# Performance work log

Measured on AMD Instinct MI355X. Metric: run time of the kernel, lower is better.

## Reference

```python
import jax, jax.numpy as jnp
import numpy as np
from jax.scipy.special import logsumexp

EPSILON = 0.01        # temperature
DIST_THRESH = 0.2
NUM_ITERS = 3
NEG_INF = -1.0e9

B, N, M, C = 4, 4096, 4096, 256


def setup_inputs() -> dict:
    key = jax.random.key(0)
    k1, k2, k3, k4, k5 = jax.random.split(key, 5)
    source_feats = jax.random.normal(k1, (B, N, C), dtype=jnp.float32)
    source_locs = jax.random.uniform(k2, (B, N, 2), dtype=jnp.float32)
    target_locs = jax.random.uniform(k3, (B, M, 2), dtype=jnp.float32)
    source_valid_mask = jax.random.bernoulli(k4, 0.9, (B, N))
    target_valid_mask = jax.random.bernoulli(k5, 0.9, (B, M))
    return {
        "source_feats": source_feats,
        "source_locs": source_locs,
        "target_locs": target_locs,
        "source_valid_mask": source_valid_mask,
        "target_valid_mask": target_valid_mask,
    }


def reference(source_feats, source_locs, target_locs, source_valid_mask, target_valid_mask):
    # pairwise squared distances: [B, M, N]
    diff = target_locs[:, :, None, :] - source_locs[:, None, :, :]  # [B, M, N, 2]
    dist_sq = jnp.sum(diff * diff, axis=-1)                          # [B, M, N]
    log_K = -dist_sq / (EPSILON + 1e-8)

    valid_connection = dist_sq < (DIST_THRESH ** 2)
    valid_connection = valid_connection & source_valid_mask[:, None, :]
    valid_connection = valid_connection & target_valid_mask[:, :, None]
    log_K = jnp.where(valid_connection, log_K, NEG_INF)

    # Sinkhorn iterations in log space
    v = jnp.zeros((log_K.shape[0], 1, log_K.shape[2]), dtype=log_K.dtype)  # [B,1,N]
    u = jnp.zeros((log_K.shape[0], log_K.shape[1], 1), dtype=log_K.dtype)  # [B,M,1]
    for _ in range(NUM_ITERS):
        u = -logsumexp(log_K + v, axis=2, keepdims=True)
        v = -logsumexp(log_K + u, axis=1, keepdims=True)
        v = jnp.where(source_valid_mask[:, None, :], v, 0.0)

    attn = jnp.exp(log_K + u + v)  # [B, M, N]
    attn = jax.lax.stop_gradient(attn)  # original computes it under torch.no_grad

    target_feats = jnp.einsum('bmn,bnc->bmc', attn, source_feats)
    target_feats = target_feats * target_valid_mask[:, :, None].astype(target_feats.dtype)
    has_source = jnp.any(valid_connection, axis=-1, keepdims=True)
    target_feats = target_feats * has_source.astype(target_feats.dtype)
    return target_feats
```

## Files before the change

kernel.cpp:

```cpp
#include <hip/hip_runtime.h>
#include <math.h>

#define BB 4
#define BN 4096
#define CC 256
constexpr float T2      = 0.04f;
constexpr float NEGINF  = -1.0e9f;
constexpr float INV_EPS = (float)(1.0 / 0.01000001);

__device__ __forceinline__ int cell_of(float x, float y) {
  int cx = (int)(x * 5.0f); cx = cx < 0 ? 0 : (cx > 4 ? 4 : cx);
  int cy = (int)(y * 5.0f); cy = cy < 0 ? 0 : (cy > 4 ? 4 : cy);
  return cy * 5 + cx;
}

__global__ void k_count(const float* __restrict__ tlocs, const float* __restrict__ slocs,
                        int* __restrict__ counts_t, int* __restrict__ counts_s) {
  int gid = blockIdx.x * 256 + threadIdx.x;
  if (gid < BB * BN) {
    int b = gid >> 12;
    atomicAdd(&counts_t[b * 32 + cell_of(tlocs[gid * 2], tlocs[gid * 2 + 1])], 1);
  } else {
    int g = gid - BB * BN;
    int b = g >> 12;
    atomicAdd(&counts_s[b * 32 + cell_of(slocs[g * 2], slocs[g * 2 + 1])], 1);
  }
}

__global__ void k_scan_scatter(const float* __restrict__ tlocs, const float* __restrict__ slocs,
                               const int* __restrict__ tmask, const int* __restrict__ smask,
                               const int* __restrict__ counts_t, const int* __restrict__ counts_s,
                               int* __restrict__ starts_t, int* __restrict__ starts_s,
                               int* __restrict__ perm_t, int* __restrict__ perm_s,
                               float4* __restrict__ t_sorted, float4* __restrict__ s_sorted) {
  const int which = blockIdx.x & 1, b = blockIdx.x >> 1;
  const float* locs = which ? slocs : tlocs;
  const int*   mask = which ? smask : tmask;
  const int* counts = which ? counts_s : counts_t;
  int* starts       = which ? starts_s : starts_t;
  int* perm         = which ? perm_s : perm_t;
  float4* pack      = which ? s_sorted : t_sorted;
  __shared__ int st[26];
  __shared__ int cur[25];
  if (threadIdx.x == 0) {
    int acc = 0;
    for (int c = 0; c < 25; c++) { st[c] = acc; acc += counts[b * 32 + c]; }
    st[25] = acc;
  }
  __syncthreads();
  if (threadIdx.x < 25) cur[threadIdx.x] = st[threadIdx.x];
  if (threadIdx.x < 26) starts[b * 32 + threadIdx.x] = st[threadIdx.x];
  __syncthreads();
  for (int i = threadIdx.x; i < BN; i += 256) {
    float x = locs[(b * BN + i) * 2], y = locs[(b * BN + i) * 2 + 1];
    int pos = atomicAdd(&cur[cell_of(x, y)], 1);
    perm[b * BN + pos] = i;
    pack[b * BN + pos] = make_float4(x, y, 0.f, mask[b * BN + i] ? 1.f : 0.f);
  }
}

__global__ __launch_bounds__(256) void k_sink(const float4* __restrict__ opp,
                                              float4* __restrict__ own,
                                              const int* __restrict__ opp_starts,
                                              const int* __restrict__ Zin,
                                              int* __restrict__ Zout,
                                              int zero_invalid) {
  const int wv   = threadIdx.x >> 6;
  const int lane = threadIdx.x & 63;
  const int rowb = blockIdx.x * 16 + wv * 4;
  const int b    = rowb >> 12;
  float4 me[4];
  float  s[4] = {0.f, 0.f, 0.f, 0.f};
  int ryLo = 5, ryHi = -1, rxLo = 5, rxHi = -1;
  #pragma unroll
  for (int i = 0; i < 4; i++) {
    me[i] = own[rowb + i];
    if (me[i].w != 0.f) {
      int cell = cell_of(me[i].x, me[i].y);
      int cy = cell / 5, cx = cell % 5;
      ryLo = min(ryLo, max(cy - 1, 0)); ryHi = max(ryHi, min(cy + 1, 4));
      rxLo = min(rxLo, max(cx - 1, 0)); rxHi = max(rxHi, min(cx + 1, 4));
    }
  }
  for (int ry = ryLo; ry <= ryHi; ry++) {
    const int r0 = opp_starts[b * 32 + ry * 5 + rxLo];
    const int r1 = opp_starts[b * 32 + ry * 5 + rxHi + 1];
    for (int j = r0 + lane; j < r1; j += 64) {
      float4 o = opp[b * BN + j];
      #pragma unroll
      for (int i = 0; i < 4; i++) {
        float dx = me[i].x - o.x, dy = me[i].y - o.y;
        float d2 = fmaf(dx, dx, dy * dy);
        bool  c  = (d2 < T2) && (o.w != 0.f) && (me[i].w != 0.f);
        float t  = c ? fmaf(d2, -INV_EPS, o.z) : -3e30f;
        s[i] += __expf(t);
      }
    }
  }
  #pragma unroll
  for (int i = 0; i < 4; i++)
    for (int off = 32; off > 0; off >>= 1) s[i] += __shfl_xor(s[i], off);
  if (lane == 0) {
    const float Zf = (float)Zin[b];
    #pragma unroll
    for (int i = 0; i < 4; i++) {
      float ss  = s[i] + Zf;
      float val = (ss > 0.f) ? -logf(ss) : 1.0e9f;
      if (zero_invalid && me[i].w == 0.f) val = 0.f;
      own[rowb + i] = make_float4(me[i].x, me[i].y, val, me[i].w);
      if (val == 1.0e9f) atomicAdd(&Zout[b], 1);
    }
  }
}

#define MAXCH 12

__global__ __launch_bounds__(256) void k_out(
    const float* __restrict__ feats, const float4* __restrict__ t_sorted,
    const float4* __restrict__ s_sorted, const int* __restrict__ perm_t,
    const int* __restrict__ perm_s, const int* __restrict__ starts_t,
    const int* __restrict__ starts_s, float* __restrict__ out) {
  const int b = blockIdx.z;
  const int cell = blockIdx.y / 3, rsel = blockIdx.y % 3;
  const int cy = cell / 5, cx = cell % 5;
  const int ry = cy + rsel - 1;
  if (ry < 0 || ry > 4) return;
  const int t0 = starts_t[b * 32 + cell], t1 = starts_t[b * 32 + cell + 1];
  const int base = t0 + blockIdx.x * 32;
  if (base >= t1) return;
  const int rx0 = max(cx - 1, 0), rx1 = min(cx + 1, 4);
  const int s0 = starts_s[b * 32 + ry * 5 + rx0];
  const int s1 = starts_s[b * 32 + ry * 5 + rx1 + 1];
  if (s0 >= s1) return;
  const int nt = min(32, t1 - base);

  __shared__ float4 tL[32];
  __shared__ int    morg[32];
  __shared__ float4 sL[16];
  __shared__ int    sorg[16];
  __shared__ __align__(16) float attnL[16][32];
  __shared__ __align__(16) float fL[16 * 256];

  const int tid = threadIdx.x;
  if (tid < 32) {
    if (tid < nt) {
      tL[tid]   = t_sorted[b * BN + base + tid];
      morg[tid] = perm_t[b * BN + base + tid];
    } else {
      tL[tid]   = make_float4(0.f, 0.f, 0.f, 0.f);
      morg[tid] = 0;
    }
  }
  const int tmg = tid >> 5;
  const int chg = tid & 31;
  float acc[4][8];
  #pragma unroll
  for (int i = 0; i < 4; i++)
    #pragma unroll
    for (int j = 0; j < 8; j++) acc[i][j] = 0.f;
  __syncthreads();

  for (int n0 = s0; n0 < s1; n0 += 16) {
    const int kk = min(16, s1 - n0);
    __syncthreads();
    if (tid < 16) {
      if (tid < kk) {
        sL[tid]   = s_sorted[b * BN + n0 + tid];
        sorg[tid] = perm_s[b * BN + n0 + tid];
      } else {
        sL[tid]   = make_float4(1e9f, 1e9f, 0.f, 0.f);
        sorg[tid] = 0;
      }
    }
    __syncthreads();
    {
      int e = tid * 2;
      #pragma unroll
      for (int q = 0; q < 2; q++, e++) {
        int nn = e >> 5, tm = e & 31;
        float4 t4 = tL[tm];
        float4 s4 = sL[nn];
        float dx = t4.x - s4.x, dy = t4.y - s4.y;
        float d2 = fmaf(dx, dx, dy * dy);
        bool  c  = (d2 < T2) && (s4.w != 0.f) && (t4.w != 0.f);
        attnL[nn][tm] = c ? __expf(fmaf(d2, -INV_EPS, t4.z + s4.z)) : 0.f;
      }
    }
    #pragma unroll
    for (int q = 0; q < 4; q++) {
      int idx = q * 256 + tid;
      ((float4*)fL)[idx] =
          ((const float4*)feats)[(((b << 12) + sorg[idx >> 6]) << 6) + (idx & 63)];
    }
    __syncthreads();
    #pragma unroll 4
    for (int nn = 0; nn < 16; nn++) {
      const float4 av = *(const float4*)&attnL[nn][tmg * 4];
      const float4 f0 = *(const float4*)&fL[nn * 256 + chg * 4];
      const float4 f1 = *(const float4*)&fL[nn * 256 + 128 + chg * 4];
      float avv[4] = {av.x, av.y, av.z, av.w};
      float ff[8]  = {f0.x, f0.y, f0.z, f0.w, f1.x, f1.y, f1.z, f1.w};
      #pragma unroll
      for (int i = 0; i < 4; i++)
        #pragma unroll
        for (int j = 0; j < 8; j++)
          acc[i][j] = fmaf(avv[i], ff[j], acc[i][j]);
    }
  }
  __syncthreads();
  #pragma unroll
  for (int i = 0; i < 4; i++) {
    int tm = tmg * 4 + i;
    if (tm < nt) {
      float* op = out + (((b << 12) + morg[tm]) << 8) + chg * 4;
      #pragma unroll
      for (int j = 0; j < 4; j++) atomicAdd(op + j,       acc[i][j]);
      #pragma unroll
      for (int j = 0; j < 4; j++) atomicAdd(op + 128 + j, acc[i][j + 4]);
    }
  }
}

extern "C" void kernel_launch(void* const* d_in, const int* in_sizes, int n_in,
                              void* d_out, int out_size, void* d_ws, size_t ws_size,
                              hipStream_t stream) {
  const float* feats = (const float*)d_in[0];
  const float* slocs = (const float*)d_in[1];
  const float* tlocs = (const float*)d_in[2];
  const int*   smask = (const int*)d_in[3];
  const int*   tmask = (const int*)d_in[4];
  float* out = (float*)d_out;

  char* ws = (char*)d_ws;
  int*    counts_t = (int*)(ws);
  int*    counts_s = (int*)(ws + 512);
  int*    Zc       = (int*)(ws + 1024);
  int*    starts_t = (int*)(ws + 2048);
  int*    starts_s = (int*)(ws + 2560);
  int*    perm_t   = (int*)(ws + 4096);
  int*    perm_s   = (int*)(ws + 69632);
  float4* s_sorted = (float4*)(ws + 135168);
  float4* t_sorted = (float4*)(ws + 397312);

  hipMemsetAsync(ws, 0, 2048, stream);
  hipMemsetAsync(out, 0, (size_t)out_size * sizeof(float), stream);
  k_count<<<128, 256, 0, stream>>>(tlocs, slocs, counts_t, counts_s);
  k_scan_scatter<<<8, 256, 0, stream>>>(tlocs, slocs, tmask, smask,
                                        counts_t, counts_s, starts_t, starts_s,
                                        perm_t, perm_s, t_sorted, s_sorted);
  for (int it = 0; it < 3; it++) {
    k_sink<<<1024, 256, 0, stream>>>(s_sorted, t_sorted, starts_s,
                                     Zc + (it == 0 ? 0 : (2 * it) * 4),
                                     Zc + (2 * it + 1) * 4, 0);
    k_sink<<<1024, 256, 0, stream>>>(t_sorted, s_sorted, starts_t,
                                     Zc + (2 * it + 1) * 4,
                                     Zc + (2 * it + 2) * 4, 1);
  }
  k_out<<<dim3(MAXCH, 75, BB), 256, 0, stream>>>(feats, t_sorted, s_sorted,
                                                 perm_t, perm_s, starts_t,
                                                 starts_s, out);
}
```

Baseline: 598.8 us.

## Fuse counting, scatter and Sinkhorn passes into one cooperative kernel

Replaces the count, scan/scatter and six Sinkhorn launches (plus a workspace memset) with a single cooperative kernel that uses grid-wide syncs between phases. This removes per-launch overhead and inter-kernel gaps. In exchange it needs all 1024 blocks co-resident for the cooperative launch, and the grid syncs add their own barrier cost. The scatter phase now runs on only 8 of the 1024 blocks while the rest wait.

```diff
diff --git a/kernel.cpp b/kernel.cpp
--- a/kernel.cpp
+++ b/kernel.cpp
@@ -1,5 +1,8 @@
 #include <hip/hip_runtime.h>
+#include <hip/hip_cooperative_groups.h>
 #include <math.h>
+
+namespace cg = cooperative_groups;
 
 #define BB 4
 #define BN 4096
@@ -14,57 +17,12 @@
   return cy * 5 + cx;
 }
 
-__global__ void k_count(const float* __restrict__ tlocs, const float* __restrict__ slocs,
-                        int* __restrict__ counts_t, int* __restrict__ counts_s) {
-  int gid = blockIdx.x * 256 + threadIdx.x;
-  if (gid < BB * BN) {
-    int b = gid >> 12;
-    atomicAdd(&counts_t[b * 32 + cell_of(tlocs[gid * 2], tlocs[gid * 2 + 1])], 1);
-  } else {
-    int g = gid - BB * BN;
-    int b = g >> 12;
-    atomicAdd(&counts_s[b * 32 + cell_of(slocs[g * 2], slocs[g * 2 + 1])], 1);
-  }
-}
-
-__global__ void k_scan_scatter(const float* __restrict__ tlocs, const float* __restrict__ slocs,
-                               const int* __restrict__ tmask, const int* __restrict__ smask,
-                               const int* __restrict__ counts_t, const int* __restrict__ counts_s,
-                               int* __restrict__ starts_t, int* __restrict__ starts_s,
-                               int* __restrict__ perm_t, int* __restrict__ perm_s,
-                               float4* __restrict__ t_sorted, float4* __restrict__ s_sorted) {
-  const int which = blockIdx.x & 1, b = blockIdx.x >> 1;
-  const float* locs = which ? slocs : tlocs;
-  const int*   mask = which ? smask : tmask;
-  const int* counts = which ? counts_s : counts_t;
-  int* starts       = which ? starts_s : starts_t;
-  int* perm         = which ? perm_s : perm_t;
-  float4* pack      = which ? s_sorted : t_sorted;
-  __shared__ int st[26];
-  __shared__ int cur[25];
-  if (threadIdx.x == 0) {
-    int acc = 0;
-    for (int c = 0; c < 25; c++) { st[c] = acc; acc += counts[b * 32 + c]; }
-    st[25] = acc;
-  }
-  __syncthreads();
-  if (threadIdx.x < 25) cur[threadIdx.x] = st[threadIdx.x];
-  if (threadIdx.x < 26) starts[b * 32 + threadIdx.x] = st[threadIdx.x];
-  __syncthreads();
-  for (int i = threadIdx.x; i < BN; i += 256) {
-    float x = locs[(b * BN + i) * 2], y = locs[(b * BN + i) * 2 + 1];
-    int pos = atomicAdd(&cur[cell_of(x, y)], 1);
-    perm[b * BN + pos] = i;
-    pack[b * BN + pos] = make_float4(x, y, 0.f, mask[b * BN + i] ? 1.f : 0.f);
-  }
-}
-
-__global__ __launch_bounds__(256) void k_sink(const float4* __restrict__ opp,
-                                              float4* __restrict__ own,
-                                              const int* __restrict__ opp_starts,
-                                              const int* __restrict__ Zin,
-                                              int* __restrict__ Zout,
-                                              int zero_invalid) {
+__device__ static void sink_pass(const float4* __restrict__ opp,
+                                 float4* __restrict__ own,
+                                 const int* __restrict__ opp_starts,
+                                 const int* __restrict__ Zin,
+                                 int* __restrict__ Zout,
+                                 int zero_invalid) {
   const int wv   = threadIdx.x >> 6;
   const int lane = threadIdx.x & 63;
   const int rowb = blockIdx.x * 16 + wv * 4;
@@ -110,6 +68,78 @@
       own[rowb + i] = make_float4(me[i].x, me[i].y, val, me[i].w);
       if (val == 1.0e9f) atomicAdd(&Zout[b], 1);
     }
+  }
+}
+
+__global__ __launch_bounds__(256) void k_fused(
+    const float* __restrict__ tlocs, const float* __restrict__ slocs,
+    const int* __restrict__ tmask, const int* __restrict__ smask,
+    int* __restrict__ wsi,
+    int* __restrict__ starts_t, int* __restrict__ starts_s,
+    int* __restrict__ perm_t, int* __restrict__ perm_s,
+    float4* __restrict__ t_sorted, float4* __restrict__ s_sorted) {
+  cg::grid_group grid = cg::this_grid();
+  int* counts_t = wsi;
+  int* counts_s = wsi + 128;
+  int* Zc       = wsi + 256;
+  const int tid  = threadIdx.x;
+  const int gtid = blockIdx.x * 256 + tid;
+
+  if (gtid < 512) wsi[gtid] = 0;
+  __threadfence();
+  grid.sync();
+
+  if (gtid < 2 * BB * BN) {
+    if (gtid < BB * BN) {
+      int b = gtid >> 12;
+      atomicAdd(&counts_t[b * 32 + cell_of(tlocs[gtid * 2], tlocs[gtid * 2 + 1])], 1);
+    } else {
+      int g = gtid - BB * BN;
+      int b = g >> 12;
+      atomicAdd(&counts_s[b * 32 + cell_of(slocs[g * 2], slocs[g * 2 + 1])], 1);
+    }
+  }
+  __threadfence();
+  grid.sync();
+
+  __shared__ int st[26];
+  __shared__ int cur[25];
+  if (blockIdx.x < 8) {
+    const int which = blockIdx.x & 1, b = blockIdx.x >> 1;
+    const float* locs = which ? slocs : tlocs;
+    const int*   mask = which ? smask : tmask;
+    const int* counts = which ? counts_s : counts_t;
+    int* starts       = which ? starts_s : starts_t;
+    int* perm         = which ? perm_s : perm_t;
+    float4* pack      = which ? s_sorted : t_sorted;
+    if (tid == 0) {
+      int acc = 0;
+      for (int c = 0; c < 25; c++) { st[c] = acc; acc += counts[b * 32 + c]; }
+      st[25] = acc;
+    }
+    __syncthreads();
+    if (tid < 25) cur[tid] = st[tid];
+    if (tid < 26) starts[b * 32 + tid] = st[tid];
+    __syncthreads();
+    for (int i = tid; i < BN; i += 256) {
+      float x = locs[(b * BN + i) * 2], y = locs[(b * BN + i) * 2 + 1];
+      int pos = atomicAdd(&cur[cell_of(x, y)], 1);
+      perm[b * BN + pos] = i;
+      pack[b * BN + pos] = make_float4(x, y, 0.f, mask[b * BN + i] ? 1.f : 0.f);
+    }
+  }
+  __threadfence();
+  grid.sync();
+
+  for (int it = 0; it < 3; it++) {
+    sink_pass(s_sorted, t_sorted, starts_s,
+              Zc + (it == 0 ? 0 : (2 * it) * 4), Zc + (2 * it + 1) * 4, 0);
+    __threadfence();
+    grid.sync();
+    sink_pass(t_sorted, s_sorted, starts_t,
+              Zc + (2 * it + 1) * 4, Zc + (2 * it + 2) * 4, 1);
+    __threadfence();
+    grid.sync();
   }
 }
 
@@ -232,9 +262,7 @@
   float* out = (float*)d_out;
 
   char* ws = (char*)d_ws;
-  int*    counts_t = (int*)(ws);
-  int*    counts_s = (int*)(ws + 512);
-  int*    Zc       = (int*)(ws + 1024);
+  int*    wsi      = (int*)(ws);
   int*    starts_t = (int*)(ws + 2048);
   int*    starts_s = (int*)(ws + 2560);
   int*    perm_t   = (int*)(ws + 4096);
@@ -242,20 +270,14 @@
   float4* s_sorted = (float4*)(ws + 135168);
   float4* t_sorted = (float4*)(ws + 397312);
 
-  hipMemsetAsync(ws, 0, 2048, stream);
   hipMemsetAsync(out, 0, (size_t)out_size * sizeof(float), stream);
-  k_count<<<128, 256, 0, stream>>>(tlocs, slocs, counts_t, counts_s);
-  k_scan_scatter<<<8, 256, 0, stream>>>(tlocs, slocs, tmask, smask,
-                                        counts_t, counts_s, starts_t, starts_s,
-                                        perm_t, perm_s, t_sorted, s_sorted);
-  for (int it = 0; it < 3; it++) {
-    k_sink<<<1024, 256, 0, stream>>>(s_sorted, t_sorted, starts_s,
-                                     Zc + (it == 0 ? 0 : (2 * it) * 4),
-                                     Zc + (2 * it + 1) * 4, 0);
-    k_sink<<<1024, 256, 0, stream>>>(t_sorted, s_sorted, starts_t,
-                                     Zc + (2 * it + 1) * 4,
-                                     Zc + (2 * it + 2) * 4, 1);
-  }
+
+  void* kargs[] = {(void*)&tlocs, (void*)&slocs, (void*)&tmask, (void*)&smask,
+                   (void*)&wsi, (void*)&starts_t, (void*)&starts_s,
+                   (void*)&perm_t, (void*)&perm_s,
+                   (void*)&t_sorted, (void*)&s_sorted};
+  hipLaunchCooperativeKernel(k_fused, dim3(1024), dim3(256), kargs, 0, stream);
+
   k_out<<<dim3(MAXCH, 75, BB), 256, 0, stream>>>(feats, t_sorted, s_sorted,
                                                  perm_t, perm_s, starts_t,
                                                  starts_s, out);
```

Result: slower. 2.073 ms (+246.2%).

## Double-buffer feature tiles with async global-to-LDS loads and fuse binning kernels

Applied to the files above, without the earlier changes.

The output kernel now double-buffers source feature rows in LDS, using global_load_lds DMA and register prefetch of the next tile's locations and permutation indices, so loads overlap the FMA accumulation. The attention tile is padded and computed directly from registers. The count and scan/scatter kernels merge into one kernel that does per-batch shared-memory counting and also zeroes Zc, which removes one launch and a memset. The cost is extra LDS (two feature buffers), which may lower occupancy, and added complexity in waitcnt and barrier handling.

```diff
diff --git a/kernel.cpp b/kernel.cpp
--- a/kernel.cpp
+++ b/kernel.cpp
@@ -5,7 +5,6 @@
 #define BN 4096
 #define CC 256
 constexpr float T2      = 0.04f;
-constexpr float NEGINF  = -1.0e9f;
 constexpr float INV_EPS = (float)(1.0 / 0.01000001);
 
 __device__ __forceinline__ int cell_of(float x, float y) {
@@ -14,44 +13,45 @@
   return cy * 5 + cx;
 }
 
-__global__ void k_count(const float* __restrict__ tlocs, const float* __restrict__ slocs,
-                        int* __restrict__ counts_t, int* __restrict__ counts_s) {
-  int gid = blockIdx.x * 256 + threadIdx.x;
-  if (gid < BB * BN) {
-    int b = gid >> 12;
-    atomicAdd(&counts_t[b * 32 + cell_of(tlocs[gid * 2], tlocs[gid * 2 + 1])], 1);
-  } else {
-    int g = gid - BB * BN;
-    int b = g >> 12;
-    atomicAdd(&counts_s[b * 32 + cell_of(slocs[g * 2], slocs[g * 2 + 1])], 1);
-  }
-}
-
-__global__ void k_scan_scatter(const float* __restrict__ tlocs, const float* __restrict__ slocs,
-                               const int* __restrict__ tmask, const int* __restrict__ smask,
-                               const int* __restrict__ counts_t, const int* __restrict__ counts_s,
-                               int* __restrict__ starts_t, int* __restrict__ starts_s,
-                               int* __restrict__ perm_t, int* __restrict__ perm_s,
-                               float4* __restrict__ t_sorted, float4* __restrict__ s_sorted) {
+__device__ __forceinline__ void dma16(const void* g, void* l) {
+  __builtin_amdgcn_global_load_lds(
+      (const __attribute__((address_space(1))) void*)g,
+      (__attribute__((address_space(3))) void*)l, 16, 0, 0);
+}
+
+__global__ __launch_bounds__(256) void k_bin(
+    const float* __restrict__ tlocs, const float* __restrict__ slocs,
+    const int* __restrict__ tmask, const int* __restrict__ smask,
+    int* __restrict__ Zc,
+    int* __restrict__ starts_t, int* __restrict__ starts_s,
+    int* __restrict__ perm_t, int* __restrict__ perm_s,
+    float4* __restrict__ t_sorted, float4* __restrict__ s_sorted) {
   const int which = blockIdx.x & 1, b = blockIdx.x >> 1;
   const float* locs = which ? slocs : tlocs;
   const int*   mask = which ? smask : tmask;
-  const int* counts = which ? counts_s : counts_t;
   int* starts       = which ? starts_s : starts_t;
   int* perm         = which ? perm_s : perm_t;
   float4* pack      = which ? s_sorted : t_sorted;
+  const int tid = threadIdx.x;
+  if (blockIdx.x == 0) Zc[tid] = 0;
+  __shared__ int cnt[25];
   __shared__ int st[26];
   __shared__ int cur[25];
-  if (threadIdx.x == 0) {
+  if (tid < 25) cnt[tid] = 0;
+  __syncthreads();
+  for (int i = tid; i < BN; i += 256)
+    atomicAdd(&cnt[cell_of(locs[(b * BN + i) * 2], locs[(b * BN + i) * 2 + 1])], 1);
+  __syncthreads();
+  if (tid == 0) {
     int acc = 0;
-    for (int c = 0; c < 25; c++) { st[c] = acc; acc += counts[b * 32 + c]; }
+    for (int c = 0; c < 25; c++) { st[c] = acc; acc += cnt[c]; }
     st[25] = acc;
   }
   __syncthreads();
-  if (threadIdx.x < 25) cur[threadIdx.x] = st[threadIdx.x];
-  if (threadIdx.x < 26) starts[b * 32 + threadIdx.x] = st[threadIdx.x];
-  __syncthreads();
-  for (int i = threadIdx.x; i < BN; i += 256) {
+  if (tid < 25) cur[tid] = st[tid];
+  if (tid < 26) starts[b * 32 + tid] = st[tid];
+  __syncthreads();
+  for (int i = tid; i < BN; i += 256) {
     float x = locs[(b * BN + i) * 2], y = locs[(b * BN + i) * 2 + 1];
     int pos = atomicAdd(&cur[cell_of(x, y)], 1);
     perm[b * BN + pos] = i;
@@ -114,6 +114,7 @@
 }
 
 #define MAXCH 12
+#define CH 16
 
 __global__ __launch_bounds__(256) void k_out(
     const float* __restrict__ feats, const float4* __restrict__ t_sorted,
@@ -136,12 +137,13 @@
 
   __shared__ float4 tL[32];
   __shared__ int    morg[32];
-  __shared__ float4 sL[16];
-  __shared__ int    sorg[16];
-  __shared__ __align__(16) float attnL[16][32];
-  __shared__ __align__(16) float fL[16 * 256];
-
-  const int tid = threadIdx.x;
+  __shared__ __align__(16) float attnL[16 * 36];
+  __shared__ __align__(16) float fL[2 * CH * 256];
+
+  const int tid  = threadIdx.x;
+  const int lane = tid & 63;
+  const int w    = tid >> 6;
+
   if (tid < 32) {
     if (tid < nt) {
       tL[tid]   = t_sorted[b * BN + base + tid];
@@ -151,53 +153,73 @@
       morg[tid] = 0;
     }
   }
-  const int tmg = tid >> 5;
-  const int chg = tid & 31;
+  __syncthreads();
+
+  const int tmg  = tid >> 5;
+  const int chg  = tid & 31;
+  const int tmp_ = w * 8 + (lane & 7);
+  const int nnA  = lane >> 3, nnB = nnA + 8;
+  const float4 t4p = tL[tmp_];
+  const int sB = b * BN;
+
+  float4 psA = s_sorted[sB + min(s0 + nnA, s1 - 1)];
+  float4 psB = s_sorted[sB + min(s0 + nnB, s1 - 1)];
+  float4 pnA, pnB;
+  int sidxN[4];
+  {
+    int s0i[4];
+    #pragma unroll
+    for (int q = 0; q < 4; q++)
+      s0i[q] = perm_s[sB + min(s0 + q * 4 + w, s1 - 1)];
+    #pragma unroll
+    for (int q = 0; q < 4; q++)
+      dma16((const char*)feats + ((size_t)((b << 12) + s0i[q]) << 10) + (size_t)lane * 16,
+            (void*)&fL[(q * 4 + w) * 256]);
+    #pragma unroll
+    for (int q = 0; q < 4; q++)
+      sidxN[q] = perm_s[sB + min(s0 + CH + q * 4 + w, s1 - 1)];
+  }
+
   float acc[4][8];
   #pragma unroll
   for (int i = 0; i < 4; i++)
     #pragma unroll
     for (int j = 0; j < 8; j++) acc[i][j] = 0.f;
-  __syncthreads();
-
-  for (int n0 = s0; n0 < s1; n0 += 16) {
-    const int kk = min(16, s1 - n0);
-    __syncthreads();
-    if (tid < 16) {
-      if (tid < kk) {
-        sL[tid]   = s_sorted[b * BN + n0 + tid];
-        sorg[tid] = perm_s[b * BN + n0 + tid];
-      } else {
-        sL[tid]   = make_float4(1e9f, 1e9f, 0.f, 0.f);
-        sorg[tid] = 0;
-      }
-    }
-    __syncthreads();
+
+  int bb = 0;
+  for (int n0 = s0; n0 < s1; n0 += CH, bb ^= 1) {
+    asm volatile("s_waitcnt vmcnt(0)" ::: "memory");
+    __builtin_amdgcn_s_barrier();
+    __builtin_amdgcn_sched_barrier(0);
+    const int n1 = n0 + CH;
+    const bool more = (n1 < s1);
+    if (more) {
+      #pragma unroll
+      for (int q = 0; q < 4; q++)
+        dma16((const char*)feats + ((size_t)((b << 12) + sidxN[q]) << 10) + (size_t)lane * 16,
+              (void*)&fL[((bb ^ 1) * CH + q * 4 + w) * 256]);
+      pnA = s_sorted[sB + min(n1 + nnA, s1 - 1)];
+      pnB = s_sorted[sB + min(n1 + nnB, s1 - 1)];
+      #pragma unroll
+      for (int q = 0; q < 4; q++)
+        sidxN[q] = perm_s[sB + min(n1 + CH + q * 4 + w, s1 - 1)];
+    }
     {
-      int e = tid * 2;
-      #pragma unroll
-      for (int q = 0; q < 2; q++, e++) {
-        int nn = e >> 5, tm = e & 31;
-        float4 t4 = tL[tm];
-        float4 s4 = sL[nn];
-        float dx = t4.x - s4.x, dy = t4.y - s4.y;
-        float d2 = fmaf(dx, dx, dy * dy);
-        bool  c  = (d2 < T2) && (s4.w != 0.f) && (t4.w != 0.f);
-        attnL[nn][tm] = c ? __expf(fmaf(d2, -INV_EPS, t4.z + s4.z)) : 0.f;
-      }
-    }
-    #pragma unroll
-    for (int q = 0; q < 4; q++) {
-      int idx = q * 256 + tid;
-      ((float4*)fL)[idx] =
-          ((const float4*)feats)[(((b << 12) + sorg[idx >> 6]) << 6) + (idx & 63)];
-    }
-    __syncthreads();
+      float dx = t4p.x - psA.x, dy = t4p.y - psA.y;
+      float d2 = fmaf(dx, dx, dy * dy);
+      bool  c  = (n0 + nnA < s1) && (d2 < T2) && (psA.w != 0.f) && (t4p.w != 0.f);
+      attnL[nnA * 36 + tmp_] = c ? __expf(fmaf(d2, -INV_EPS, t4p.z + psA.z)) : 0.f;
+      dx = t4p.x - psB.x; dy = t4p.y - psB.y;
+      d2 = fmaf(dx, dx, dy * dy);
+      c  = (n0 + nnB < s1) && (d2 < T2) && (psB.w != 0.f) && (t4p.w != 0.f);
+      attnL[nnB * 36 + tmp_] = c ? __expf(fmaf(d2, -INV_EPS, t4p.z + psB.z)) : 0.f;
+    }
+    const float* fb = &fL[bb * CH * 256];
     #pragma unroll 4
     for (int nn = 0; nn < 16; nn++) {
-      const float4 av = *(const float4*)&attnL[nn][tmg * 4];
-      const float4 f0 = *(const float4*)&fL[nn * 256 + chg * 4];
-      const float4 f1 = *(const float4*)&fL[nn * 256 + 128 + chg * 4];
+      const float4 av = *(const float4*)&attnL[nn * 36 + tmg * 4];
+      const float4 f0 = *(const float4*)&fb[nn * 256 + chg * 4];
+      const float4 f1 = *(const float4*)&fb[nn * 256 + 128 + chg * 4];
       float avv[4] = {av.x, av.y, av.z, av.w};
       float ff[8]  = {f0.x, f0.y, f0.z, f0.w, f1.x, f1.y, f1.z, f1.w};
       #pragma unroll
@@ -206,8 +228,8 @@
         for (int j = 0; j < 8; j++)
           acc[i][j] = fmaf(avv[i], ff[j], acc[i][j]);
     }
-  }
-  __syncthreads();
+    if (more) { psA = pnA; psB = pnB; }
+  }
   #pragma unroll
   for (int i = 0; i < 4; i++) {
     int tm = tmg * 4 + i;
@@ -232,8 +254,6 @@
   float* out = (float*)d_out;
 
   char* ws = (char*)d_ws;
-  int*    counts_t = (int*)(ws);
-  int*    counts_s = (int*)(ws + 512);
   int*    Zc       = (int*)(ws + 1024);
   int*    starts_t = (int*)(ws + 2048);
   int*    starts_s = (int*)(ws + 2560);
@@ -242,12 +262,10 @@
   float4* s_sorted = (float4*)(ws + 135168);
   float4* t_sorted = (float4*)(ws + 397312);
 
-  hipMemsetAsync(ws, 0, 2048, stream);
   hipMemsetAsync(out, 0, (size_t)out_size * sizeof(float), stream);
-  k_count<<<128, 256, 0, stream>>>(tlocs, slocs, counts_t, counts_s);
-  k_scan_scatter<<<8, 256, 0, stream>>>(tlocs, slocs, tmask, smask,
-                                        counts_t, counts_s, starts_t, starts_s,
-                                        perm_t, perm_s, t_sorted, s_sorted);
+  k_bin<<<8, 256, 0, stream>>>(tlocs, slocs, tmask, smask, Zc,
+                               starts_t, starts_s, perm_t, perm_s,
+                               t_sorted, s_sorted);
   for (int it = 0; it < 3; it++) {
     k_sink<<<1024, 256, 0, stream>>>(s_sorted, t_sorted, starts_s,
                                      Zc + (it == 0 ? 0 : (2 * it) * 4),
```

After: 572.4 us. 1.05x faster.
